# Kernel tuning notes

Measured on AMD Instinct MI355X. Metric: run time of the kernel, lower is better.

Reference implementation:

```python
import jax, jax.numpy as jnp
import numpy as np
from math import sqrt

B, H, S, D = 4, 16, 2048, 64
NEG = -1000000000.0

def setup_inputs() -> dict:
    key = jax.random.key(0)
    kq, kk, kv, km = jax.random.split(key, 4)
    Q = jax.random.normal(kq, (B, H, S, D), dtype=jnp.float32)
    K = jax.random.normal(kk, (B, H, S, D), dtype=jnp.float32)
    V = jax.random.normal(kv, (B, H, S, D), dtype=jnp.float32)
    mask = jax.random.uniform(km, (B, 1, S, S)) < 0.1
    return {"Q": Q, "K": K, "V": V, "mask": mask}

def reference(Q, K, V, mask) -> jnp.ndarray:
    # scores: [B,H,S,S]
    scores = jnp.einsum('bhqd,bhkd->bhqk', Q, K)
    scores = jnp.where(mask, NEG, scores)
    attn = jax.nn.softmax(scores / sqrt(Q.shape[-1]), axis=-1)
    return jnp.einsum('bhqk,bhkd->bhqd', attn, V)
```

## Files before the change

### kernel.cpp

```cpp
#include <hip/hip_runtime.h>


#define SEQ 2048
#define DIM 64
#define NBH 64
#define LOG2E 1.44269504088896340736f
#define SCL (0.125f * LOG2E)
#define NEG_SCALED -1.25e8f

typedef short bf16x8 __attribute__((ext_vector_type(8)));
typedef float f32x4 __attribute__((ext_vector_type(4)));
typedef float f32x16 __attribute__((ext_vector_type(16)));

static __device__ __forceinline__ unsigned short f2bf(float f) {
    unsigned int u = __float_as_uint(f);
    u += 0x7fffu + ((u >> 16) & 1u);
    return (unsigned short)(u >> 16);
}

#define GLD16(gp, lp) __builtin_amdgcn_global_load_lds( \
    (const __attribute__((address_space(1))) unsigned int*)(gp), \
    (__attribute__((address_space(3))) unsigned int*)(lp), 16, 0, 0)

__global__ __launch_bounds__(256)
void prep_all_kernel(const float* __restrict__ K, const float* __restrict__ V,
                     const int* __restrict__ M,
                     unsigned short* __restrict__ Kb, unsigned short* __restrict__ Vt,
                     unsigned int* __restrict__ Mpt) {
    const int x = blockIdx.x;
    const int t = threadIdx.x;
    if (x < 1024) {
        __shared__ unsigned int Wt[64][8];
        const int m  = x;
        const int b  = m >> 8;
        const int q0 = ((m >> 3) & 31) * 64;
        const int k0 = (m & 7) * 256;
        const int w  = t >> 6, l = t & 63;
        #pragma unroll 4
        for (int row = 0; row < 16; ++row) {
            const int q = q0 + w * 16 + row;
            int4 v4 = *(const int4*)(M + ((size_t)b * SEQ + q) * SEQ + k0 + l * 4);
            unsigned int nib = (unsigned int)(v4.x != 0) | ((unsigned int)(v4.y != 0) << 1)
                             | ((unsigned int)(v4.z != 0) << 2) | ((unsigned int)(v4.w != 0) << 3);
            unsigned int v = nib << (4 * (l & 7));
            v |= __shfl_xor(v, 1);
            v |= __shfl_xor(v, 2);
            v |= __shfl_xor(v, 4);
            if ((l & 7) == 0) Wt[w * 16 + row][l >> 3] = v;
        }
        __syncthreads();
        {
            const int q = t & 63, g0 = t >> 6;
            #pragma unroll
            for (int gg = 0; gg < 2; ++gg) {
                const int g = g0 + gg * 4;
                Mpt[((size_t)b * 64 + (k0 >> 5) + g) * SEQ + q0 + q] = Wt[q][g];
            }
        }
    } else if (x < 5120) {
        size_t i0 = ((size_t)(x - 1024) * 256 + t) * 8;
        float4 a = *(const float4*)(K + i0);
        float4 b = *(const float4*)(K + i0 + 4);
        union { uint4 u; unsigned short s[8]; } w;
        w.s[0] = f2bf(a.x); w.s[1] = f2bf(a.y); w.s[2] = f2bf(a.z); w.s[3] = f2bf(a.w);
        w.s[4] = f2bf(b.x); w.s[5] = f2bf(b.y); w.s[6] = f2bf(b.z); w.s[7] = f2bf(b.w);
        *(uint4*)(Kb + i0) = w.u;
    } else {
        __shared__ __align__(16) unsigned short T[64 * 64];
        const int vb = x - 5120;
        const int bh = vb >> 5;
        const int k0 = (vb & 31) * 64;
        {
            const float* Vb = V + ((size_t)bh * SEQ + k0) * DIM;
            #pragma unroll
            for (int j = 0; j < 4; ++j) {
                const int fi = (j * 256 + t) * 4;
                const int kk = fi >> 6;
                const int d0 = fi & 63;
                float4 f = *(const float4*)(Vb + fi);
                const int u  = (kk & ~12) | ((kk & 4) << 1) | ((kk & 8) >> 1);
                const int cs = (d0 >> 4) ^ ((u >> 3) & 3);
                union { uint2 q; unsigned short s[4]; } w4;
                w4.s[0] = f2bf(f.x); w4.s[1] = f2bf(f.y);
                w4.s[2] = f2bf(f.z); w4.s[3] = f2bf(f.w);
                *(uint2*)&T[u * 64 + cs * 16 + (d0 & 15)] = w4.q;
            }
        }
        __syncthreads();
        {
            const int kc = t & 7;
            const int dp = t >> 3;
            const int ch = (dp >> 3) ^ (kc & 3);
            const unsigned int* T32 = (const unsigned int*)T;
            union { uint4 u; unsigned short s[8]; } o0, o1;
            #pragma unroll
            for (int i = 0; i < 8; ++i) {
                unsigned int v = T32[(8 * kc + i) * 32 + ch * 8 + (dp & 7)];
                o0.s[i] = (unsigned short)v;
                o1.s[i] = (unsigned short)(v >> 16);
            }
            unsigned short* op = Vt + ((size_t)bh * DIM + 2 * dp) * SEQ + k0 + 8 * kc;
            *(uint4*)op         = o0.u;
            *(uint4*)(op + SEQ) = o1.u;
        }
    }
}


#define TILE_QK(sc, Ktb, mqv)                                                   \
    {                                                                           \
        _Pragma("unroll")                                                       \
        for (int r = 0; r < 16; ++r) {                                          \
            const int s_ = (r & 3) + 8 * (r >> 2);                              \
            sc[r] = __int_as_float(__builtin_amdgcn_sbfe(mqv, s_, 1) & 0xC2C80000u); \
        }                                                                       \
        __builtin_amdgcn_s_setprio(1);                                          \
        _Pragma("unroll")                                                       \
        for (int dc = 0; dc < 4; ++dc) {                                        \
            const int pos = (dc * 2 + h) ^ (q32 & 7);                           \
            bf16x8 kf = *(const bf16x8*)((Ktb) + q32 * 64 + pos * 8);           \
            sc = __builtin_amdgcn_mfma_f32_32x32x16_bf16(kf, qf[dc], sc, 0, 0, 0); \
        }                                                                       \
        __builtin_amdgcn_s_setprio(0);                                          \
    }

#define TILE_SMPV(sc, Vsb)                                                      \
    {                                                                           \
        float pv_[16];                                                          \
        _Pragma("unroll")                                                       \
        for (int r = 0; r < 16; ++r) pv_[r] = __builtin_amdgcn_exp2f(sc[r]);    \
        _Pragma("unroll")                                                       \
        for (int r = 0; r < 16; r += 4) {                                       \
            ls0 += pv_[r + 0]; ls1 += pv_[r + 1];                               \
            ls2 += pv_[r + 2]; ls3 += pv_[r + 3];                               \
        }                                                                       \
        unsigned int pk_[8];                                                    \
        _Pragma("unroll")                                                       \
        for (int m = 0; m < 8; ++m)                                             \
            asm("v_cvt_pk_bf16_f32 %0, %1, %2"                                  \
                : "=v"(pk_[m]) : "v"(pv_[2 * m]), "v"(pv_[2 * m + 1]));         \
        __builtin_amdgcn_s_setprio(1);                                          \
        _Pragma("unroll")                                                       \
        for (int kk = 0; kk < 2; ++kk) {                                        \
            union { unsigned int u[4]; bf16x8 v; } fr;                          \
            fr.u[0] = pk_[4 * kk + 0]; fr.u[1] = pk_[4 * kk + 1];               \
            fr.u[2] = pk_[4 * kk + 2]; fr.u[3] = pk_[4 * kk + 3];               \
            _Pragma("unroll")                                                   \
            for (int dh = 0; dh < 2; ++dh) {                                    \
                const int d = dh * 32 + q32;                                    \
                const int pos = (kk * 2 + h) ^ ((q32 >> 1) & 3);                \
                bf16x8 vf = *(const bf16x8*)((Vsb) + d * 32 + pos * 8);         \
                acc[dh] = __builtin_amdgcn_mfma_f32_32x32x16_bf16(vf, fr.v, acc[dh], 0, 0, 0); \
            }                                                                   \
        }                                                                       \
        __builtin_amdgcn_s_setprio(0);                                          \
    }

__global__ __launch_bounds__(256, 4)
void attn_main_kernel(const float* __restrict__ Q,
                      const unsigned short* __restrict__ Kb,
                      const unsigned short* __restrict__ Vt,
                      const unsigned int* __restrict__ Mpt,
                      float* __restrict__ O)
{
    const int n    = blockIdx.y * gridDim.x + blockIdx.x;
    const int bh   = ((n & 7) << 3) | (n >> 7);
    const int q0   = ((n >> 3) & 15) * 128;
    const int b    = bh >> 4;
    const int tid  = threadIdx.x;
    const int wave = tid >> 6;
    const int lane = tid & 63;
    const int h    = lane >> 5;
    const int q32  = lane & 31;
    const int sh4  = 4 * h;

    __shared__ __align__(16) unsigned short Kt[2][2][32 * 64];
    __shared__ __align__(16) unsigned short Vs[2][2][64 * 32];

    const unsigned short* Kbh = Kb + (size_t)bh * SEQ * DIM;
    const unsigned short* Vbh = Vt + (size_t)bh * SEQ * DIM;

    bf16x8 qf[4];
    {
        const float* qp = Q + ((size_t)bh * SEQ + q0 + wave * 32 + q32) * DIM + h * 8;
        #pragma unroll
        for (int dc = 0; dc < 4; ++dc) {
            float4 xx = *(const float4*)(qp + dc * 16);
            float4 yy = *(const float4*)(qp + dc * 16 + 4);
            qf[dc][0] = (short)f2bf(xx.x * SCL); qf[dc][1] = (short)f2bf(xx.y * SCL);
            qf[dc][2] = (short)f2bf(xx.z * SCL); qf[dc][3] = (short)f2bf(xx.w * SCL);
            qf[dc][4] = (short)f2bf(yy.x * SCL); qf[dc][5] = (short)f2bf(yy.y * SCL);
            qf[dc][6] = (short)f2bf(yy.z * SCL); qf[dc][7] = (short)f2bf(yy.w * SCL);
        }
    }

    const int kkey  = wave * 8 + (lane >> 3);
    const int kclog = (lane & 7) ^ (lane >> 3);
    const unsigned short* kg = Kbh + (size_t)kkey * DIM + kclog * 8;
    const int vd    = wave * 16 + (lane >> 2);
    const int vclog = (lane & 3) ^ ((lane >> 3) & 3);
    const unsigned short* vg = Vbh + (size_t)vd * SEQ + vclog * 8;
    unsigned short* kl0 = &Kt[0][0][wave * 512];
    unsigned short* vl0 = &Vs[0][0][wave * 512];

    const unsigned int* mp = Mpt + (size_t)b * 64 * SEQ + (q0 + wave * 32 + q32);

    f32x16 acc[2];
    #pragma unroll
    for (int i = 0; i < 16; ++i) { acc[0][i] = 0.f; acc[1][i] = 0.f; }
    float ls0 = 0.f, ls1 = 0.f, ls2 = 0.f, ls3 = 0.f;

    GLD16(kg,                     kl0);
    GLD16(kg + (size_t)32 * DIM,  kl0 + 2048);
    GLD16(vg,                     vl0);
    GLD16(vg + 32,                vl0 + 2048);
    unsigned int mw0 = mp[0];
    unsigned int mw1 = mp[SEQ];

    #pragma unroll 2
    for (int g = 0; g < SEQ / 64; ++g) {
        __syncthreads();

        unsigned int mwn0 = 0, mwn1 = 0;
        if (g + 1 < SEQ / 64) {
            const size_t ko = (size_t)(g + 1) * 64 * DIM;
            const size_t vo = (size_t)(g + 1) * 64;
            const int nb = (g + 1) & 1;
            GLD16(kg + ko,                 kl0 + nb * 4096);
            GLD16(kg + ko + 32 * DIM,      kl0 + nb * 4096 + 2048);
            GLD16(vg + vo,                 vl0 + nb * 4096);
            GLD16(vg + vo + 32,            vl0 + nb * 4096 + 2048);
            mwn0 = mp[(2 * g + 2) * SEQ];
            mwn1 = mp[(2 * g + 3) * SEQ];
        }

        const int cb = g & 1;
        const unsigned short* Kt0 = &Kt[cb][0][0];
        const unsigned short* Kt1 = &Kt[cb][1][0];
        const unsigned short* Vs0 = &Vs[cb][0][0];
        const unsigned short* Vs1 = &Vs[cb][1][0];
        const unsigned int mq0 = mw0 >> sh4;
        const unsigned int mq1 = mw1 >> sh4;

        f32x16 sc0, sc1;
        TILE_QK(sc0, Kt0, mq0);
        TILE_QK(sc1, Kt1, mq1);
        TILE_SMPV(sc0, Vs0);
        TILE_SMPV(sc1, Vs1);

        mw0 = mwn0; mw1 = mwn1;
    }

    float lsum = (ls0 + ls1) + (ls2 + ls3);
    lsum += __shfl_xor(lsum, 32);
    const float inv = 1.f / lsum;
    float* orow = O + ((size_t)bh * SEQ + q0 + wave * 32 + q32) * DIM;
    #pragma unroll
    for (int dh = 0; dh < 2; ++dh) {
        #pragma unroll
        for (int r23 = 0; r23 < 4; ++r23) {
            float4 w;
            w.x = acc[dh][4 * r23 + 0] * inv;
            w.y = acc[dh][4 * r23 + 1] * inv;
            w.z = acc[dh][4 * r23 + 2] * inv;
            w.w = acc[dh][4 * r23 + 3] * inv;
            *(float4*)(orow + dh * 32 + r23 * 8 + h * 4) = w;
        }
    }
}

__global__ __launch_bounds__(256)
void attn_fallback_kernel(const float* __restrict__ Q,
                          const float* __restrict__ K,
                          const float* __restrict__ V,
                          const int* __restrict__ mask,
                          float* __restrict__ O)
{
    const int bh   = blockIdx.y;
    const int b    = bh >> 4;
    const int q0   = blockIdx.x * 64;
    const int tid  = threadIdx.x;
    const int wave = tid >> 6;
    const int lane = tid & 63;
    const int quad = lane >> 4;
    const int l16  = lane & 15;

    __shared__ __align__(16) unsigned short Klds[32][72];
    __shared__ __align__(16) unsigned short VT[64][40];
    __shared__ __align__(16) unsigned short Plds[4][16][40];

    const float* Qb = Q + (size_t)bh * SEQ * DIM;
    const float* Kb = K + (size_t)bh * SEQ * DIM;
    const float* Vb = V + (size_t)bh * SEQ * DIM;
    const int*   Mb = mask + (size_t)b * SEQ * SEQ;

    const int qrow_frag = q0 + wave * 16 + l16;
    bf16x8 qf0, qf1;
    {
        const float* qp = Qb + (size_t)qrow_frag * DIM + quad * 8;
        #pragma unroll
        for (int i = 0; i < 8; ++i) {
            qf0[i] = (short)f2bf(qp[i]);
            qf1[i] = (short)f2bf(qp[32 + i]);
        }
    }

    f32x4 acc[4];
    #pragma unroll
    for (int dg = 0; dg < 4; ++dg) acc[dg] = (f32x4){0.f, 0.f, 0.f, 0.f};
    float mrowv[4] = {-INFINITY, -INFINITY, -INFINITY, -INFINITY};
    float lrow[4] = {0.f, 0.f, 0.f, 0.f};

    const int skey = tid >> 3;
    const int sd0  = (tid & 7) * 8;
    const int vkey = tid & 31;
    const int vd0  = (tid >> 5) * 8;
    const int qrow_m = q0 + wave * 16 + quad * 4;

    for (int kb = 0; kb < SEQ; kb += 32) {
        __syncthreads();
        {
            const float* kp = Kb + (size_t)(kb + skey) * DIM + sd0;
            union { uint4 u4; unsigned short s[8]; } kw;
            #pragma unroll
            for (int i = 0; i < 8; ++i) kw.s[i] = f2bf(kp[i]);
            *(uint4*)&Klds[skey][sd0] = kw.u4;
        }
        {
            const float* vp = Vb + (size_t)(kb + vkey) * DIM + vd0;
            #pragma unroll
            for (int i = 0; i < 8; ++i) VT[vd0 + i][vkey] = f2bf(vp[i]);
        }
        __syncthreads();

        f32x4 scr[2];
        scr[0] = (f32x4){0.f, 0.f, 0.f, 0.f};
        scr[1] = (f32x4){0.f, 0.f, 0.f, 0.f};
        #pragma unroll
        for (int nt = 0; nt < 2; ++nt) {
            bf16x8 kf0 = *(const bf16x8*)&Klds[nt * 16 + l16][quad * 8];
            bf16x8 kf1 = *(const bf16x8*)&Klds[nt * 16 + l16][32 + quad * 8];
            scr[nt] = __builtin_amdgcn_mfma_f32_16x16x32_bf16(qf0, kf0, scr[nt], 0, 0, 0);
            scr[nt] = __builtin_amdgcn_mfma_f32_16x16x32_bf16(qf1, kf1, scr[nt], 0, 0, 0);
        }

        float x[2][4];
        #pragma unroll
        for (int nt = 0; nt < 2; ++nt)
            #pragma unroll
            for (int r = 0; r < 4; ++r) {
                int mv = Mb[(size_t)(qrow_m + r) * SEQ + kb + nt * 16 + l16];
                x[nt][r] = mv ? NEG_SCALED : scr[nt][r] * 0.125f;
            }

        float p[2][4];
        #pragma unroll
        for (int r = 0; r < 4; ++r) {
            float rm = fmaxf(x[0][r], x[1][r]);
            #pragma unroll
            for (int off = 1; off < 16; off <<= 1)
                rm = fmaxf(rm, __shfl_xor(rm, off, 16));
            float mn = fmaxf(mrowv[r], rm);
            float alpha = exp2f((mrowv[r] - mn) * LOG2E);
            mrowv[r] = mn;
            float p0 = exp2f((x[0][r] - mn) * LOG2E);
            float p1 = exp2f((x[1][r] - mn) * LOG2E);
            p[0][r] = p0; p[1][r] = p1;
            float rs = p0 + p1;
            #pragma unroll
            for (int off = 1; off < 16; off <<= 1)
                rs += __shfl_xor(rs, off, 16);
            lrow[r] = lrow[r] * alpha + rs;
            #pragma unroll
            for (int dg = 0; dg < 4; ++dg)
                acc[dg][r] *= alpha;
        }

        #pragma unroll
        for (int nt = 0; nt < 2; ++nt)
            #pragma unroll
            for (int r = 0; r < 4; ++r)
                Plds[wave][quad * 4 + r][nt * 16 + l16] = f2bf(p[nt][r]);

        bf16x8 pf = *(const bf16x8*)&Plds[wave][l16][quad * 8];

        #pragma unroll
        for (int dg = 0; dg < 4; ++dg) {
            bf16x8 vf = *(const bf16x8*)&VT[dg * 16 + l16][quad * 8];
            acc[dg] = __builtin_amdgcn_mfma_f32_16x16x32_bf16(pf, vf, acc[dg], 0, 0, 0);
        }
    }

    float* Ob = O + (size_t)bh * SEQ * DIM;
    #pragma unroll
    for (int r = 0; r < 4; ++r) {
        float inv = 1.f / lrow[r];
        #pragma unroll
        for (int dg = 0; dg < 4; ++dg)
            Ob[(size_t)(qrow_m + r) * DIM + dg * 16 + l16] = acc[dg][r] * inv;
    }
}

extern "C" void kernel_launch(void* const* d_in, const int* in_sizes, int n_in,
                              void* d_out, int out_size, void* d_ws, size_t ws_size,
                              hipStream_t stream) {
    const float* Q = (const float*)d_in[0];
    const float* K = (const float*)d_in[1];
    const float* V = (const float*)d_in[2];
    const int* mask = (const int*)d_in[3];
    float*        O = (float*)d_out;

    const size_t szK = (size_t)NBH * SEQ * DIM * 2;
    const size_t szV = (size_t)NBH * SEQ * DIM * 2;
    const size_t szM = (size_t)4 * SEQ * (SEQ / 32) * 4;
    const size_t need = szK + szV + szM;

    if (ws_size >= need) {
        unsigned short* Kb = (unsigned short*)d_ws;
        unsigned short* Vt = (unsigned short*)((char*)d_ws + szK);
        unsigned int*  Mpt = (unsigned int*)((char*)d_ws + szK + szV);

        prep_all_kernel<<<dim3(7168), 256, 0, stream>>>(K, V, mask, Kb, Vt, Mpt);
        attn_main_kernel<<<dim3(SEQ / 128, NBH), 256, 0, stream>>>(Q, Kb, Vt, Mpt, O);
    } else {
        attn_fallback_kernel<<<dim3(SEQ / 64, NBH), 256, 0, stream>>>(Q, K, V, mask, O);
    }
}
```

Measured before the change: 271.4 us.

## Pre-swizzle K and V into MFMA-fragment-order blobs per 64-key tile

The prep kernel now writes K and V for each 64-key tile into one contiguous 16KB blob, already laid out in the exact per-lane MFMA fragment order. The main kernel loads each blob with straight contiguous global-to-LDS copies and reads fragments at fixed offsets, with no XOR swizzle address math. The packed mask is interleaved so both 32-key mask words come from a single 8-byte load. This cuts address arithmetic and uses simpler, more coalesced loads. The cost is that fragments are read from LDS in a linear lane order, which could cause bank conflicts, and the prep kernel's K pass now does a strided gather.

Result: no change. 267.3 us (-1.5%).

```diff
diff --git a/kernel.cpp b/kernel.cpp
--- a/kernel.cpp
+++ b/kernel.cpp
@@ -25,8 +25,7 @@
 __global__ __launch_bounds__(256)
 void prep_all_kernel(const float* __restrict__ K, const float* __restrict__ V,
                      const int* __restrict__ M,
-                     unsigned short* __restrict__ Kb, unsigned short* __restrict__ Vt,
-                     unsigned int* __restrict__ Mpt) {
+                     unsigned short* __restrict__ Fb, unsigned int* __restrict__ Mpt) {
     const int x = blockIdx.x;
     const int t = threadIdx.x;
     if (x < 1024) {
@@ -54,22 +53,38 @@
             #pragma unroll
             for (int gg = 0; gg < 2; ++gg) {
                 const int g = g0 + gg * 4;
-                Mpt[((size_t)b * 64 + (k0 >> 5) + g) * SEQ + q0 + q] = Wt[q][g];
+                const int G = (k0 >> 5) + g;
+                Mpt[(((size_t)b * 32 + (G >> 1)) * SEQ + q0 + q) * 2 + (G & 1)] = Wt[q][g];
             }
         }
-    } else if (x < 5120) {
-        size_t i0 = ((size_t)(x - 1024) * 256 + t) * 8;
-        float4 a = *(const float4*)(K + i0);
-        float4 b = *(const float4*)(K + i0 + 4);
-        union { uint4 u; unsigned short s[8]; } w;
-        w.s[0] = f2bf(a.x); w.s[1] = f2bf(a.y); w.s[2] = f2bf(a.z); w.s[3] = f2bf(a.w);
-        w.s[4] = f2bf(b.x); w.s[5] = f2bf(b.y); w.s[6] = f2bf(b.z); w.s[7] = f2bf(b.w);
-        *(uint4*)(Kb + i0) = w.u;
+    } else if (x < 3072) {
+        const int kb = x - 1024;
+        const int bh = kb >> 5;
+        const int g  = kb & 31;
+        const float* Kg = K + ((size_t)bh * SEQ + g * 64) * DIM;
+        unsigned short* Fo = Fb + (((size_t)bh * 32 + g) * 8192);
+        #pragma unroll
+        for (int i = 0; i < 2; ++i) {
+            const int u   = i * 256 + t;
+            const int sub = u >> 8;
+            const int dc  = (u >> 6) & 3;
+            const int ln  = u & 63;
+            const int hh  = ln >> 5;
+            const int q32 = ln & 31;
+            const float* kp = Kg + (size_t)(sub * 32 + q32) * DIM + dc * 16 + hh * 8;
+            float4 a = *(const float4*)kp;
+            float4 b2 = *(const float4*)(kp + 4);
+            union { uint4 q4; unsigned short s[8]; } w;
+            w.s[0] = f2bf(a.x); w.s[1] = f2bf(a.y); w.s[2] = f2bf(a.z); w.s[3] = f2bf(a.w);
+            w.s[4] = f2bf(b2.x); w.s[5] = f2bf(b2.y); w.s[6] = f2bf(b2.z); w.s[7] = f2bf(b2.w);
+            *(uint4*)(Fo + (size_t)u * 8) = w.q4;
+        }
     } else {
         __shared__ __align__(16) unsigned short T[64 * 64];
-        const int vb = x - 5120;
+        const int vb = x - 3072;
         const int bh = vb >> 5;
-        const int k0 = (vb & 31) * 64;
+        const int g  = vb & 31;
+        const int k0 = g * 64;
         {
             const float* Vb = V + ((size_t)bh * SEQ + k0) * DIM;
             #pragma unroll
@@ -88,26 +103,34 @@
         }
         __syncthreads();
         {
-            const int kc = t & 7;
-            const int dp = t >> 3;
-            const int ch = (dp >> 3) ^ (kc & 3);
+            const int p   = t & 31;
+            const int w2  = t >> 5;
+            const int sub = w2 >> 2;
+            const int kk  = (w2 >> 1) & 1;
+            const int hh  = w2 & 1;
+            const int dh  = p >> 4;
+            const int q32a = (2 * p) & 31;
+            const int ub  = sub * 32 + kk * 16 + hh * 8;
             const unsigned int* T32 = (const unsigned int*)T;
-            union { uint4 u; unsigned short s[8]; } o0, o1;
-            #pragma unroll
-            for (int i = 0; i < 8; ++i) {
-                unsigned int v = T32[(8 * kc + i) * 32 + ch * 8 + (dp & 7)];
-                o0.s[i] = (unsigned short)v;
-                o1.s[i] = (unsigned short)(v >> 16);
+            union { uint4 q4; unsigned short s[8]; } o0, o1;
+            #pragma unroll
+            for (int j = 0; j < 8; ++j) {
+                const int u  = ub + j;
+                const int ch = (p >> 3) ^ ((u >> 3) & 3);
+                unsigned int v = T32[u * 32 + ch * 8 + (p & 7)];
+                o0.s[j] = (unsigned short)v;
+                o1.s[j] = (unsigned short)(v >> 16);
             }
-            unsigned short* op = Vt + ((size_t)bh * DIM + 2 * dp) * SEQ + k0 + 8 * kc;
-            *(uint4*)op         = o0.u;
-            *(uint4*)(op + SEQ) = o1.u;
+            unsigned short* dst = Fb + (((size_t)bh * 32 + g) * 8192) + 4096
+                                + sub * 2048 + kk * 1024 + dh * 512 + hh * 256 + q32a * 8;
+            *(uint4*)dst       = o0.q4;
+            *(uint4*)(dst + 8) = o1.q4;
         }
     }
 }
 
 
-#define TILE_QK(sc, Ktb, mqv)                                                   \
+#define TILE_QK(sc, sub, mqv)                                                   \
     {                                                                           \
         _Pragma("unroll")                                                       \
         for (int r = 0; r < 16; ++r) {                                          \
@@ -117,14 +140,13 @@
         __builtin_amdgcn_s_setprio(1);                                          \
         _Pragma("unroll")                                                       \
         for (int dc = 0; dc < 4; ++dc) {                                        \
-            const int pos = (dc * 2 + h) ^ (q32 & 7);                           \
-            bf16x8 kf = *(const bf16x8*)((Ktb) + q32 * 64 + pos * 8);           \
+            bf16x8 kf = *(const bf16x8*)(Bl + (sub) * 2048 + dc * 512);         \
             sc = __builtin_amdgcn_mfma_f32_32x32x16_bf16(kf, qf[dc], sc, 0, 0, 0); \
         }                                                                       \
         __builtin_amdgcn_s_setprio(0);                                          \
     }
 
-#define TILE_SMPV(sc, Vsb)                                                      \
+#define TILE_SMPV(sc, sub)                                                      \
     {                                                                           \
         float pv_[16];                                                          \
         _Pragma("unroll")                                                       \
@@ -147,9 +169,7 @@
             fr.u[2] = pk_[4 * kk + 2]; fr.u[3] = pk_[4 * kk + 3];               \
             _Pragma("unroll")                                                   \
             for (int dh = 0; dh < 2; ++dh) {                                    \
-                const int d = dh * 32 + q32;                                    \
-                const int pos = (kk * 2 + h) ^ ((q32 >> 1) & 3);                \
-                bf16x8 vf = *(const bf16x8*)((Vsb) + d * 32 + pos * 8);         \
+                bf16x8 vf = *(const bf16x8*)(Bl + 4096 + (sub) * 2048 + kk * 1024 + dh * 512); \
                 acc[dh] = __builtin_amdgcn_mfma_f32_32x32x16_bf16(vf, fr.v, acc[dh], 0, 0, 0); \
             }                                                                   \
         }                                                                       \
@@ -158,8 +178,7 @@
 
 __global__ __launch_bounds__(256, 4)
 void attn_main_kernel(const float* __restrict__ Q,
-                      const unsigned short* __restrict__ Kb,
-                      const unsigned short* __restrict__ Vt,
+                      const unsigned short* __restrict__ Fb,
                       const unsigned int* __restrict__ Mpt,
                       float* __restrict__ O)
 {
@@ -174,11 +193,9 @@
     const int q32  = lane & 31;
     const int sh4  = 4 * h;
 
-    __shared__ __align__(16) unsigned short Kt[2][2][32 * 64];
-    __shared__ __align__(16) unsigned short Vs[2][2][64 * 32];
-
-    const unsigned short* Kbh = Kb + (size_t)bh * SEQ * DIM;
-    const unsigned short* Vbh = Vt + (size_t)bh * SEQ * DIM;
+    __shared__ __align__(16) unsigned short Blob[2][8192];
+
+    const unsigned short* Fbh = Fb + (size_t)bh * 32 * 8192;
 
     bf16x8 qf[4];
     {
@@ -194,61 +211,45 @@
         }
     }
 
-    const int kkey  = wave * 8 + (lane >> 3);
-    const int kclog = (lane & 7) ^ (lane >> 3);
-    const unsigned short* kg = Kbh + (size_t)kkey * DIM + kclog * 8;
-    const int vd    = wave * 16 + (lane >> 2);
-    const int vclog = (lane & 3) ^ ((lane >> 3) & 3);
-    const unsigned short* vg = Vbh + (size_t)vd * SEQ + vclog * 8;
-    unsigned short* kl0 = &Kt[0][0][wave * 512];
-    unsigned short* vl0 = &Vs[0][0][wave * 512];
-
-    const unsigned int* mp = Mpt + (size_t)b * 64 * SEQ + (q0 + wave * 32 + q32);
+    const unsigned short* fg = Fbh + wave * 2048 + lane * 8;
+
+    const unsigned int* mp = Mpt + ((size_t)b * 32 * SEQ + q0 + wave * 32 + q32) * 2;
 
     f32x16 acc[2];
     #pragma unroll
     for (int i = 0; i < 16; ++i) { acc[0][i] = 0.f; acc[1][i] = 0.f; }
     float ls0 = 0.f, ls1 = 0.f, ls2 = 0.f, ls3 = 0.f;
 
-    GLD16(kg,                     kl0);
-    GLD16(kg + (size_t)32 * DIM,  kl0 + 2048);
-    GLD16(vg,                     vl0);
-    GLD16(vg + 32,                vl0 + 2048);
-    unsigned int mw0 = mp[0];
-    unsigned int mw1 = mp[SEQ];
+    #pragma unroll
+    for (int c = 0; c < 4; ++c)
+        GLD16(fg + c * 512, &Blob[0][wave * 2048 + c * 512]);
+    uint2 mwp = *(const uint2*)mp;
 
     #pragma unroll 2
     for (int g = 0; g < SEQ / 64; ++g) {
         __syncthreads();
 
-        unsigned int mwn0 = 0, mwn1 = 0;
+        uint2 mwpn = {0u, 0u};
         if (g + 1 < SEQ / 64) {
-            const size_t ko = (size_t)(g + 1) * 64 * DIM;
-            const size_t vo = (size_t)(g + 1) * 64;
+            const unsigned short* fgn = fg + (size_t)(g + 1) * 8192;
             const int nb = (g + 1) & 1;
-            GLD16(kg + ko,                 kl0 + nb * 4096);
-            GLD16(kg + ko + 32 * DIM,      kl0 + nb * 4096 + 2048);
-            GLD16(vg + vo,                 vl0 + nb * 4096);
-            GLD16(vg + vo + 32,            vl0 + nb * 4096 + 2048);
-            mwn0 = mp[(2 * g + 2) * SEQ];
-            mwn1 = mp[(2 * g + 3) * SEQ];
-        }
-
-        const int cb = g & 1;
-        const unsigned short* Kt0 = &Kt[cb][0][0];
-        const unsigned short* Kt1 = &Kt[cb][1][0];
-        const unsigned short* Vs0 = &Vs[cb][0][0];
-        const unsigned short* Vs1 = &Vs[cb][1][0];
-        const unsigned int mq0 = mw0 >> sh4;
-        const unsigned int mq1 = mw1 >> sh4;
+            #pragma unroll
+            for (int c = 0; c < 4; ++c)
+                GLD16(fgn + c * 512, &Blob[nb][wave * 2048 + c * 512]);
+            mwpn = *(const uint2*)(mp + (size_t)(g + 1) * 2 * SEQ);
+        }
+
+        const unsigned short* Bl = &Blob[g & 1][0] + lane * 8;
+        const unsigned int mq0 = mwp.x >> sh4;
+        const unsigned int mq1 = mwp.y >> sh4;
 
         f32x16 sc0, sc1;
-        TILE_QK(sc0, Kt0, mq0);
-        TILE_QK(sc1, Kt1, mq1);
-        TILE_SMPV(sc0, Vs0);
-        TILE_SMPV(sc1, Vs1);
-
-        mw0 = mwn0; mw1 = mwn1;
+        TILE_QK(sc0, 0, mq0);
+        TILE_QK(sc1, 1, mq1);
+        TILE_SMPV(sc0, 0);
+        TILE_SMPV(sc1, 1);
+
+        mwp = mwpn;
     }
 
     float lsum = (ls0 + ls1) + (ls2 + ls3);
@@ -410,18 +411,16 @@
     const int* mask = (const int*)d_in[3];
     float*        O = (float*)d_out;
 
-    const size_t szK = (size_t)NBH * SEQ * DIM * 2;
-    const size_t szV = (size_t)NBH * SEQ * DIM * 2;
+    const size_t szF = (size_t)NBH * 32 * 8192 * 2;
     const size_t szM = (size_t)4 * SEQ * (SEQ / 32) * 4;
-    const size_t need = szK + szV + szM;
+    const size_t need = szF + szM;
 
     if (ws_size >= need) {
-        unsigned short* Kb = (unsigned short*)d_ws;
-        unsigned short* Vt = (unsigned short*)((char*)d_ws + szK);
-        unsigned int*  Mpt = (unsigned int*)((char*)d_ws + szK + szV);
-
-        prep_all_kernel<<<dim3(7168), 256, 0, stream>>>(K, V, mask, Kb, Vt, Mpt);
-        attn_main_kernel<<<dim3(SEQ / 128, NBH), 256, 0, stream>>>(Q, Kb, Vt, Mpt, O);
+        unsigned short* Fb = (unsigned short*)d_ws;
+        unsigned int*  Mpt = (unsigned int*)((char*)d_ws + szF);
+
+        prep_all_kernel<<<dim3(5120), 256, 0, stream>>>(K, V, mask, Fb, Mpt);
+        attn_main_kernel<<<dim3(SEQ / 128, NBH), 256, 0, stream>>>(Q, Fb, Mpt, O);
     } else {
         attn_fallback_kernel<<<dim3(SEQ / 64, NBH), 256, 0, stream>>>(Q, K, V, mask, O);
     }
```
